# Kernel optimization log

Measured on AMD Instinct MI355X. Metric: run time of the kernel, lower is better.

## Reference

```python
import jax, jax.numpy as jnp
import numpy as np

SCALE = 8.0  # sqrt(hid=64), passed as init arg `scale`


def setup_inputs() -> dict:
    key = jax.random.key(0)
    kq, kk, kv, km = jax.random.split(key, 4)
    B, S, H = 32, 2048, 64  # B = bs*n_head
    q = jax.random.normal(kq, (B, S, H), dtype=jnp.float32)
    k = jax.random.normal(kk, (B, S, H), dtype=jnp.float32)
    v = jax.random.normal(kv, (B, S, H), dtype=jnp.float32)
    mask = jax.random.bernoulli(km, 0.1, (B, S, S))  # True = masked out
    return {"q": q, "k": k, "v": v, "mask": mask, "cca": 0}


def reference(q, k, v, mask, cca):
    # scores: [B, Sq, Sk]
    attn = jnp.einsum('bqh,bkh->bqk', q, k) / SCALE
    if mask is not None:
        attn = jnp.where(mask, jnp.finfo(q.dtype).min, attn)
    if cca:
        # CCA branch: softmax over the query/sequence axis (dim=1)
        attn = jax.nn.softmax(attn, axis=1)
        ctx = jnp.einsum('bq,bkh->bqh', attn.squeeze(-1)[..., None].squeeze(-1), v) if attn.ndim == 2 else jnp.einsum('bqk,bkh->bqh', attn, v)
    else:
        attn = jax.nn.softmax(attn, axis=2)
        ctx = jnp.einsum('bqk,bkh->bqh', attn, v)  # [B, Sq, H]
    return (ctx, attn)
```

## Files before the change

kernel.cpp:

```cpp
#include <hip/hip_runtime.h>
#include <hip/hip_bf16.h>

typedef __bf16    bf16x8_t __attribute__((ext_vector_type(8)));
typedef float     f32x4_t  __attribute__((ext_vector_type(4)));
typedef short     s16x4_t  __attribute__((ext_vector_type(4)));
typedef short     s16x8_t  __attribute__((ext_vector_type(8)));
typedef unsigned  u32x4_t  __attribute__((ext_vector_type(4)));

#define S_LEN 2048
#define HDIM  64
#define BQ    32
#define NTHREADS 1024
#define PSTR_B 4112
#define BMSTR 264

__device__ __forceinline__ short f2bf(float f) {
    return __builtin_bit_cast(short, (__bf16)f);
}
__device__ __forceinline__ float bf2f(short s) {
    return __builtin_bit_cast(float, ((unsigned)(unsigned short)s) << 16);
}
__device__ __forceinline__ short* pelem(short* P, int row, int e) {
    return (short*)((char*)P + (unsigned)row * PSTR_B + (unsigned)e * 2u);
}
__device__ __forceinline__ const short* pelemc(const short* P, int row, int e) {
    return pelem(const_cast<short*>(P), row, e);
}
__device__ __forceinline__ unsigned nzmask16(u32x4_t w) {
    unsigned n = 0;
    #pragma unroll
    for (int i = 0; i < 4; ++i) {
        const unsigned x = w[i];
        const unsigned t = (x & 0x7F7F7F7Fu) + 0x7F7F7F7Fu;
        const unsigned z = ((t | x) & 0x80808080u) >> 7;
        n |= ((z * 0x10204081u) >> 28) << (4 * i);
    }
    return n;
}
__device__ __forceinline__ unsigned nzmask4w(u32x4_t w) {
    return (w[0] ? 1u : 0u) | (w[1] ? 2u : 0u) | (w[2] ? 4u : 0u) | (w[3] ? 8u : 0u);
}

#define PK8(lo, hi, out8) { s16x8_t _t; \
    _t[0]=f2bf((lo)[0]); _t[1]=f2bf((lo)[1]); _t[2]=f2bf((lo)[2]); _t[3]=f2bf((lo)[3]); \
    _t[4]=f2bf((hi)[0]); _t[5]=f2bf((hi)[1]); _t[6]=f2bf((hi)[2]); _t[7]=f2bf((hi)[3]); \
    (out8) = __builtin_bit_cast(bf16x8_t, _t); }
#define PKV(src, dst) { s16x8_t _t; \
    _t[0]=f2bf((src)[0]); _t[1]=f2bf((src)[1]); _t[2]=f2bf((src)[2]); _t[3]=f2bf((src)[3]); \
    _t[4]=f2bf((src)[4]); _t[5]=f2bf((src)[5]); _t[6]=f2bf((src)[6]); _t[7]=f2bf((src)[7]); \
    (dst) = __builtin_bit_cast(bf16x8_t, _t); }

__global__ void detect_mask(const unsigned char* __restrict__ M, int* __restrict__ flags) {
    __shared__ int cnt[4];
    if (threadIdx.x < 4) cnt[threadIdx.x] = 0;
    __syncthreads();
    int local[4] = {0, 0, 0, 0};
    for (int i = threadIdx.x; i < 16384; i += 256)
        if (M[i]) local[i & 3]++;
    #pragma unroll
    for (int c = 0; c < 4; ++c)
        if (local[c]) atomicAdd(&cnt[c], local[c]);
    __syncthreads();
    if (threadIdx.x == 0) {
        int stride;
        if (cnt[1] == 0 && cnt[2] == 0 && cnt[3] == 0)      stride = 4;
        else if (cnt[0] == 0 && cnt[1] == 0)                stride = 4;
        else                                                stride = 1;
        flags[0] = stride;
    }
}

__global__ __launch_bounds__(NTHREADS, 1)
void sdpa_one(const float* __restrict__ Q, const float* __restrict__ K,
              const float* __restrict__ V, const unsigned char* __restrict__ M,
              const int* __restrict__ MF, float* __restrict__ OUT)
{
    __shared__ short Plds[BQ * (PSTR_B / 2)];
    __shared__ unsigned char Bm[BQ * BMSTR];
    __shared__ float Pvx[BQ][HDIM];
    __shared__ float rowsum[BQ];
    __shared__ float rinv_s[BQ];

    const int tid  = threadIdx.x;
    const int w    = tid >> 6;
    const int lane = tid & 63;
    const int col  = lane & 15;
    const int kg   = lane >> 4;
    const int mstride = MF[0];

    const int id   = blockIdx.x;
    const int slot = id >> 3;
    const int b    = ((slot >> 6) << 3) | (id & 7);
    const int q0   = (slot & 63) * BQ;

    float* attn_out = OUT + (size_t)32 * S_LEN * HDIM;

    if (tid < BQ) rowsum[tid] = 0.f;
    {
        float* pz = &Pvx[0][0];
        pz[tid] = 0.f;
        pz[tid + 1024] = 0.f;
    }

    {
        const int row  = tid >> 5;
        const int segE = (tid & 31) * 64;
        unsigned long long bits = 0ull;
        if (mstride == 1) {
            const unsigned char* mp = M + (size_t)b * S_LEN * S_LEN
                                        + (size_t)(q0 + row) * S_LEN + segE;
            #pragma unroll
            for (int j = 0; j < 4; ++j)
                bits |= (unsigned long long)nzmask16(*(const u32x4_t*)(mp + j * 16))
                        << (16 * j);
        } else {
            const unsigned* mp = (const unsigned*)M + (size_t)b * S_LEN * S_LEN
                                   + (size_t)(q0 + row) * S_LEN + segE;
            #pragma unroll
            for (int j = 0; j < 16; ++j)
                bits |= (unsigned long long)nzmask4w(*(const u32x4_t*)(mp + j * 4))
                        << (4 * j);
        }
        *(unsigned long long*)&Bm[row * BMSTR + (segE >> 3)] = bits;
    }

    bf16x8_t af[2][2];
    #pragma unroll
    for (int m = 0; m < 2; ++m)
        #pragma unroll
        for (int kk = 0; kk < 2; ++kk) {
            const float* qp = Q + ((size_t)b * S_LEN + q0 + m * 16 + col) * HDIM + kk * 32 + kg * 8;
            const f32x4_t qa = *(const f32x4_t*)qp;
            const f32x4_t qb = *(const f32x4_t*)(qp + 4);
            PK8(qa, qb, af[m][kk]);
        }
    __syncthreads();

    float rs0 = 0.f, rs1 = 0.f;
    {
        const float* Kb = K + (size_t)b * S_LEN * HDIM;
        f32x4_t A0,B0,C0,D0, A1,B1,C1,D1;
#define LDK(f, AX,BX,CX,DX) { \
    const float* kp = Kb + (size_t)(w * 128 + (f) * 16 + col) * HDIM + kg * 8; \
    AX = *(const f32x4_t*)kp;        BX = *(const f32x4_t*)(kp + 4); \
    CX = *(const f32x4_t*)(kp + 32); DX = *(const f32x4_t*)(kp + 36); }
#define STEP(f, AX,BX,CX,DX, PF, fp) { \
    bf16x8_t kb0, kb1; PK8(AX, BX, kb0); PK8(CX, DX, kb1); \
    if (PF) LDK(fp, AX,BX,CX,DX); \
    f32x4_t acc0 = {0.f,0.f,0.f,0.f}, acc1 = {0.f,0.f,0.f,0.f}; \
    acc0 = __builtin_amdgcn_mfma_f32_16x16x32_bf16(kb0, af[0][0], acc0, 0,0,0); \
    acc0 = __builtin_amdgcn_mfma_f32_16x16x32_bf16(kb1, af[0][1], acc0, 0,0,0); \
    acc1 = __builtin_amdgcn_mfma_f32_16x16x32_bf16(kb0, af[1][0], acc1, 0,0,0); \
    acc1 = __builtin_amdgcn_mfma_f32_16x16x32_bf16(kb1, af[1][1], acc1, 0,0,0); \
    const int c0 = w * 128 + (f) * 16 + kg * 4; \
    const int sh = c0 & 7; \
    { const unsigned bb = Bm[col * BMSTR + (c0 >> 3)]; \
      float p0 = ((bb >> (sh    )) & 1u) ? 0.f : __expf(acc0[0] * 0.125f); \
      float p1 = ((bb >> (sh + 1)) & 1u) ? 0.f : __expf(acc0[1] * 0.125f); \
      float p2 = ((bb >> (sh + 2)) & 1u) ? 0.f : __expf(acc0[2] * 0.125f); \
      float p3 = ((bb >> (sh + 3)) & 1u) ? 0.f : __expf(acc0[3] * 0.125f); \
      rs0 += (p0 + p1) + (p2 + p3); \
      s16x4_t pk; pk[0]=f2bf(p0); pk[1]=f2bf(p1); pk[2]=f2bf(p2); pk[3]=f2bf(p3); \
      *(s16x4_t*)pelem(Plds, col, c0) = pk; } \
    { const unsigned bb = Bm[(16 + col) * BMSTR + (c0 >> 3)]; \
      float p0 = ((bb >> (sh    )) & 1u) ? 0.f : __expf(acc1[0] * 0.125f); \
      float p1 = ((bb >> (sh + 1)) & 1u) ? 0.f : __expf(acc1[1] * 0.125f); \
      float p2 = ((bb >> (sh + 2)) & 1u) ? 0.f : __expf(acc1[2] * 0.125f); \
      float p3 = ((bb >> (sh + 3)) & 1u) ? 0.f : __expf(acc1[3] * 0.125f); \
      rs1 += (p0 + p1) + (p2 + p3); \
      s16x4_t pk; pk[0]=f2bf(p0); pk[1]=f2bf(p1); pk[2]=f2bf(p2); pk[3]=f2bf(p3); \
      *(s16x4_t*)pelem(Plds, 16 + col, c0) = pk; } }
        LDK(0, A0,B0,C0,D0);
        LDK(1, A1,B1,C1,D1);
        #pragma unroll
        for (int ff = 0; ff < 8; ff += 2) {
            STEP(ff,     A0,B0,C0,D0, (ff + 2 < 8), ff + 2);
            STEP(ff + 1, A1,B1,C1,D1, (ff + 3 < 8), ff + 3);
        }
#undef LDK
#undef STEP
    }
    {
        float s0 = rs0, s1 = rs1;
        s0 += __shfl_xor(s0, 16); s0 += __shfl_xor(s0, 32);
        s1 += __shfl_xor(s1, 16); s1 += __shfl_xor(s1, 32);
        if (lane < 16) {
            atomicAdd(&rowsum[col], s0);
            atomicAdd(&rowsum[16 + col], s1);
        }
    }
    __syncthreads();
    if (tid < BQ) rinv_s[tid] = 1.0f / rowsum[tid];
    __syncthreads();

    const int hb    = (w & 3) * 16;
    const int kbase = (w >> 2) * 512;
    const float* Vb = V + (size_t)b * S_LEN * HDIM;

    f32x4_t cacc0 = {0.f,0.f,0.f,0.f}, cacc1 = {0.f,0.f,0.f,0.f};
    {
        float vr0[8], vr1[8];
#define LOADV(kc, dst) { \
    const float* vp = Vb + (size_t)(kbase + (kc) * 32 + kg * 8) * HDIM + hb + col; \
    dst[0] = vp[0];        dst[1] = vp[HDIM];     dst[2] = vp[2*HDIM]; dst[3] = vp[3*HDIM]; \
    dst[4] = vp[4*HDIM];   dst[5] = vp[5*HDIM];   dst[6] = vp[6*HDIM]; dst[7] = vp[7*HDIM]; }
#define PVSTEP(kc, vsrc) { \
    bf16x8_t vbf; PKV(vsrc, vbf); \
    const int ke = kbase + (kc) * 32 + kg * 8; \
    const bf16x8_t pa0 = *(const bf16x8_t*)pelemc(Plds, col,      ke); \
    const bf16x8_t pa1 = *(const bf16x8_t*)pelemc(Plds, 16 + col, ke); \
    cacc0 = __builtin_amdgcn_mfma_f32_16x16x32_bf16(pa0, vbf, cacc0, 0,0,0); \
    cacc1 = __builtin_amdgcn_mfma_f32_16x16x32_bf16(pa1, vbf, cacc1, 0,0,0); }
        LOADV(0, vr0); LOADV(1, vr1);
        #pragma unroll
        for (int kc = 0; kc < 14; kc += 2) {
            PVSTEP(kc,     vr0); LOADV(kc + 2, vr0);
            PVSTEP(kc + 1, vr1); LOADV(kc + 3, vr1);
        }
        PVSTEP(14, vr0);
        PVSTEP(15, vr1);
#undef LOADV
#undef PVSTEP
    }
    #pragma unroll
    for (int r = 0; r < 4; ++r) {
        atomicAdd(&Pvx[kg * 4 + r][hb + col],      cacc0[r]);
        atomicAdd(&Pvx[16 + kg * 4 + r][hb + col], cacc1[r]);
    }

    {
        const int srow = w * 2 + (lane >> 5);
        const int lc   = lane & 31;
        const float my_rinv = rinv_s[srow];
        float* abp = attn_out + ((size_t)b * S_LEN + q0 + srow) * S_LEN + lc * 4;
        #pragma unroll 4
        for (int sec = 0; sec < 16; ++sec) {
            const s16x4_t pv = *(const s16x4_t*)pelemc(Plds, srow, sec * 128 + lc * 4);
            f32x4_t o;
            o[0] = bf2f(pv[0]) * my_rinv; o[1] = bf2f(pv[1]) * my_rinv;
            o[2] = bf2f(pv[2]) * my_rinv; o[3] = bf2f(pv[3]) * my_rinv;
            *(f32x4_t*)(abp + sec * 128) = o;
        }
    }

    __syncthreads();
    {
        const int row = tid >> 5;
        const int c0  = (tid & 31) * 2;
        const float ri = rinv_s[row];
        float2 o;
        o.x = Pvx[row][c0]     * ri;
        o.y = Pvx[row][c0 + 1] * ri;
        *(float2*)(OUT + ((size_t)b * S_LEN + q0 + row) * HDIM + c0) = o;
    }
}

extern "C" void kernel_launch(void* const* d_in, const int* in_sizes, int n_in,
                              void* d_out, int out_size, void* d_ws, size_t ws_size,
                              hipStream_t stream)
{
    const float* q = (const float*)d_in[0];
    const float* k = (const float*)d_in[1];
    const float* v = (const float*)d_in[2];
    const unsigned char* mask = (const unsigned char*)d_in[3];
    int* mflags = (int*)d_ws;
    float* out = (float*)d_out;
    detect_mask<<<dim3(1), dim3(256), 0, stream>>>(mask, mflags);
    sdpa_one<<<dim3(2048), dim3(NTHREADS), 0, stream>>>(q, k, v, mask, mflags, out);
}
```

Baseline: 451.7 us.

## Pre-convert K and V to bf16 in a separate pass and vectorize mask bit reads

Adds a to_bf16 kernel that converts K and V to bf16 once into workspace, so the attention kernel loads half the bytes and skips per-block conversion. Each K/V row is reused by 64 query blocks, so the conversion is amortized. The per-step mask byte lookups become two 16-byte LDS loads per wave, with the mask stride padded to 272. The cost is an extra kernel launch plus a full write and read of the converted buffers, and K prefetch pipelining is dropped in favour of direct loads.

```diff
diff --git a/kernel.cpp b/kernel.cpp
--- a/kernel.cpp
+++ b/kernel.cpp
@@ -12,7 +12,8 @@
 #define BQ    32
 #define NTHREADS 1024
 #define PSTR_B 4112
-#define BMSTR 264
+#define BMSTR 272
+#define KV_ELEMS (32 * S_LEN * HDIM)
 
 __device__ __forceinline__ short f2bf(float f) {
     return __builtin_bit_cast(short, (__bf16)f);
@@ -40,15 +41,6 @@
 __device__ __forceinline__ unsigned nzmask4w(u32x4_t w) {
     return (w[0] ? 1u : 0u) | (w[1] ? 2u : 0u) | (w[2] ? 4u : 0u) | (w[3] ? 8u : 0u);
 }
-
-#define PK8(lo, hi, out8) { s16x8_t _t; \
-    _t[0]=f2bf((lo)[0]); _t[1]=f2bf((lo)[1]); _t[2]=f2bf((lo)[2]); _t[3]=f2bf((lo)[3]); \
-    _t[4]=f2bf((hi)[0]); _t[5]=f2bf((hi)[1]); _t[6]=f2bf((hi)[2]); _t[7]=f2bf((hi)[3]); \
-    (out8) = __builtin_bit_cast(bf16x8_t, _t); }
-#define PKV(src, dst) { s16x8_t _t; \
-    _t[0]=f2bf((src)[0]); _t[1]=f2bf((src)[1]); _t[2]=f2bf((src)[2]); _t[3]=f2bf((src)[3]); \
-    _t[4]=f2bf((src)[4]); _t[5]=f2bf((src)[5]); _t[6]=f2bf((src)[6]); _t[7]=f2bf((src)[7]); \
-    (dst) = __builtin_bit_cast(bf16x8_t, _t); }
 
 __global__ void detect_mask(const unsigned char* __restrict__ M, int* __restrict__ flags) {
     __shared__ int cnt[4];
@@ -70,9 +62,23 @@
     }
 }
 
+__global__ __launch_bounds__(256)
+void to_bf16(const float* __restrict__ K, const float* __restrict__ V,
+             short* __restrict__ Kb, short* __restrict__ Vb)
+{
+    const size_t i = ((size_t)blockIdx.x * 256 + threadIdx.x) * 4;
+    const f32x4_t k4 = *(const f32x4_t*)(K + i);
+    const f32x4_t v4 = *(const f32x4_t*)(V + i);
+    s16x4_t ks, vs;
+    ks[0] = f2bf(k4[0]); ks[1] = f2bf(k4[1]); ks[2] = f2bf(k4[2]); ks[3] = f2bf(k4[3]);
+    vs[0] = f2bf(v4[0]); vs[1] = f2bf(v4[1]); vs[2] = f2bf(v4[2]); vs[3] = f2bf(v4[3]);
+    *(s16x4_t*)(Kb + i) = ks;
+    *(s16x4_t*)(Vb + i) = vs;
+}
+
 __global__ __launch_bounds__(NTHREADS, 1)
-void sdpa_one(const float* __restrict__ Q, const float* __restrict__ K,
-              const float* __restrict__ V, const unsigned char* __restrict__ M,
+void sdpa_one(const float* __restrict__ Q, const short* __restrict__ Kbf,
+              const short* __restrict__ Vbf, const unsigned char* __restrict__ M,
               const int* __restrict__ MF, float* __restrict__ OUT)
 {
     __shared__ short Plds[BQ * (PSTR_B / 2)];
@@ -132,52 +138,46 @@
             const float* qp = Q + ((size_t)b * S_LEN + q0 + m * 16 + col) * HDIM + kk * 32 + kg * 8;
             const f32x4_t qa = *(const f32x4_t*)qp;
             const f32x4_t qb = *(const f32x4_t*)(qp + 4);
-            PK8(qa, qb, af[m][kk]);
-        }
-    __syncthreads();
+            s16x8_t t;
+            t[0]=f2bf(qa[0]); t[1]=f2bf(qa[1]); t[2]=f2bf(qa[2]); t[3]=f2bf(qa[3]);
+            t[4]=f2bf(qb[0]); t[5]=f2bf(qb[1]); t[6]=f2bf(qb[2]); t[7]=f2bf(qb[3]);
+            af[m][kk] = __builtin_bit_cast(bf16x8_t, t);
+        }
+    __syncthreads();
+
+    const u32x4_t mw0 = *(const u32x4_t*)&Bm[col * BMSTR + w * 16];
+    const u32x4_t mw1 = *(const u32x4_t*)&Bm[(16 + col) * BMSTR + w * 16];
 
     float rs0 = 0.f, rs1 = 0.f;
     {
-        const float* Kb = K + (size_t)b * S_LEN * HDIM;
-        f32x4_t A0,B0,C0,D0, A1,B1,C1,D1;
-#define LDK(f, AX,BX,CX,DX) { \
-    const float* kp = Kb + (size_t)(w * 128 + (f) * 16 + col) * HDIM + kg * 8; \
-    AX = *(const f32x4_t*)kp;        BX = *(const f32x4_t*)(kp + 4); \
-    CX = *(const f32x4_t*)(kp + 32); DX = *(const f32x4_t*)(kp + 36); }
-#define STEP(f, AX,BX,CX,DX, PF, fp) { \
-    bf16x8_t kb0, kb1; PK8(AX, BX, kb0); PK8(CX, DX, kb1); \
-    if (PF) LDK(fp, AX,BX,CX,DX); \
+        const short* Kb = Kbf + (size_t)b * S_LEN * HDIM;
+#define STEP(f) { \
+    const short* kp_ = Kb + (size_t)(w * 128 + (f) * 16 + col) * HDIM + kg * 8; \
+    const bf16x8_t kb0 = *(const bf16x8_t*)kp_; \
+    const bf16x8_t kb1 = *(const bf16x8_t*)(kp_ + 32); \
     f32x4_t acc0 = {0.f,0.f,0.f,0.f}, acc1 = {0.f,0.f,0.f,0.f}; \
     acc0 = __builtin_amdgcn_mfma_f32_16x16x32_bf16(kb0, af[0][0], acc0, 0,0,0); \
     acc0 = __builtin_amdgcn_mfma_f32_16x16x32_bf16(kb1, af[0][1], acc0, 0,0,0); \
     acc1 = __builtin_amdgcn_mfma_f32_16x16x32_bf16(kb0, af[1][0], acc1, 0,0,0); \
     acc1 = __builtin_amdgcn_mfma_f32_16x16x32_bf16(kb1, af[1][1], acc1, 0,0,0); \
     const int c0 = w * 128 + (f) * 16 + kg * 4; \
-    const int sh = c0 & 7; \
-    { const unsigned bb = Bm[col * BMSTR + (c0 >> 3)]; \
-      float p0 = ((bb >> (sh    )) & 1u) ? 0.f : __expf(acc0[0] * 0.125f); \
-      float p1 = ((bb >> (sh + 1)) & 1u) ? 0.f : __expf(acc0[1] * 0.125f); \
-      float p2 = ((bb >> (sh + 2)) & 1u) ? 0.f : __expf(acc0[2] * 0.125f); \
-      float p3 = ((bb >> (sh + 3)) & 1u) ? 0.f : __expf(acc0[3] * 0.125f); \
+    const unsigned bb0 = mw0[(f) >> 1] >> (((f) & 1) * 16 + kg * 4); \
+    const unsigned bb1 = mw1[(f) >> 1] >> (((f) & 1) * 16 + kg * 4); \
+    { float p0 = (bb0      & 1u) ? 0.f : __expf(acc0[0] * 0.125f); \
+      float p1 = ((bb0>>1) & 1u) ? 0.f : __expf(acc0[1] * 0.125f); \
+      float p2 = ((bb0>>2) & 1u) ? 0.f : __expf(acc0[2] * 0.125f); \
+      float p3 = ((bb0>>3) & 1u) ? 0.f : __expf(acc0[3] * 0.125f); \
       rs0 += (p0 + p1) + (p2 + p3); \
       s16x4_t pk; pk[0]=f2bf(p0); pk[1]=f2bf(p1); pk[2]=f2bf(p2); pk[3]=f2bf(p3); \
       *(s16x4_t*)pelem(Plds, col, c0) = pk; } \
-    { const unsigned bb = Bm[(16 + col) * BMSTR + (c0 >> 3)]; \
-      float p0 = ((bb >> (sh    )) & 1u) ? 0.f : __expf(acc1[0] * 0.125f); \
-      float p1 = ((bb >> (sh + 1)) & 1u) ? 0.f : __expf(acc1[1] * 0.125f); \
-      float p2 = ((bb >> (sh + 2)) & 1u) ? 0.f : __expf(acc1[2] * 0.125f); \
-      float p3 = ((bb >> (sh + 3)) & 1u) ? 0.f : __expf(acc1[3] * 0.125f); \
+    { float p0 = (bb1      & 1u) ? 0.f : __expf(acc1[0] * 0.125f); \
+      float p1 = ((bb1>>1) & 1u) ? 0.f : __expf(acc1[1] * 0.125f); \
+      float p2 = ((bb1>>2) & 1u) ? 0.f : __expf(acc1[2] * 0.125f); \
+      float p3 = ((bb1>>3) & 1u) ? 0.f : __expf(acc1[3] * 0.125f); \
       rs1 += (p0 + p1) + (p2 + p3); \
       s16x4_t pk; pk[0]=f2bf(p0); pk[1]=f2bf(p1); pk[2]=f2bf(p2); pk[3]=f2bf(p3); \
       *(s16x4_t*)pelem(Plds, 16 + col, c0) = pk; } }
-        LDK(0, A0,B0,C0,D0);
-        LDK(1, A1,B1,C1,D1);
-        #pragma unroll
-        for (int ff = 0; ff < 8; ff += 2) {
-            STEP(ff,     A0,B0,C0,D0, (ff + 2 < 8), ff + 2);
-            STEP(ff + 1, A1,B1,C1,D1, (ff + 3 < 8), ff + 3);
-        }
-#undef LDK
+        STEP(0) STEP(1) STEP(2) STEP(3) STEP(4) STEP(5) STEP(6) STEP(7)
 #undef STEP
     }
     {
@@ -195,17 +195,17 @@
 
     const int hb    = (w & 3) * 16;
     const int kbase = (w >> 2) * 512;
-    const float* Vb = V + (size_t)b * S_LEN * HDIM;
+    const short* Vb = Vbf + (size_t)b * S_LEN * HDIM;
 
     f32x4_t cacc0 = {0.f,0.f,0.f,0.f}, cacc1 = {0.f,0.f,0.f,0.f};
     {
-        float vr0[8], vr1[8];
+        s16x8_t vr0, vr1;
 #define LOADV(kc, dst) { \
-    const float* vp = Vb + (size_t)(kbase + (kc) * 32 + kg * 8) * HDIM + hb + col; \
+    const short* vp = Vb + (size_t)(kbase + (kc) * 32 + kg * 8) * HDIM + hb + col; \
     dst[0] = vp[0];        dst[1] = vp[HDIM];     dst[2] = vp[2*HDIM]; dst[3] = vp[3*HDIM]; \
     dst[4] = vp[4*HDIM];   dst[5] = vp[5*HDIM];   dst[6] = vp[6*HDIM]; dst[7] = vp[7*HDIM]; }
 #define PVSTEP(kc, vsrc) { \
-    bf16x8_t vbf; PKV(vsrc, vbf); \
+    const bf16x8_t vbf = __builtin_bit_cast(bf16x8_t, vsrc); \
     const int ke = kbase + (kc) * 32 + kg * 8; \
     const bf16x8_t pa0 = *(const bf16x8_t*)pelemc(Plds, col,      ke); \
     const bf16x8_t pa1 = *(const bf16x8_t*)pelemc(Plds, 16 + col, ke); \
@@ -263,8 +263,13 @@
     const float* k = (const float*)d_in[1];
     const float* v = (const float*)d_in[2];
     const unsigned char* mask = (const unsigned char*)d_in[3];
-    int* mflags = (int*)d_ws;
     float* out = (float*)d_out;
+
+    int*   mflags = (int*)d_ws;
+    short* kbf = (short*)((char*)d_ws + (1 << 20));
+    short* vbf = kbf + KV_ELEMS;
+
     detect_mask<<<dim3(1), dim3(256), 0, stream>>>(mask, mflags);
-    sdpa_one<<<dim3(2048), dim3(NTHREADS), 0, stream>>>(q, k, v, mask, mflags, out);
-}
+    to_bf16<<<dim3(KV_ELEMS / 4 / 256), dim3(256), 0, stream>>>(k, v, kbf, vbf);
+    sdpa_one<<<dim3(2048), dim3(NTHREADS), 0, stream>>>(q, kbf, vbf, mask, mflags, out);
+}
```

Result: faster. 407.1 us (-9.9%).
